# Optimization experiments

Hardware: AMD Instinct MI355X
Metric: run time of the kernel (lower is better)

Reference implementation:

```python
import jax, jax.numpy as jnp
import numpy as np

B, R, C, O, I = 256, 1152, 10, 16, 8  # batch, routes, digit caps, out dim, in dim


def conv2d(x, w, b, stride, pad):
    y = jax.lax.conv_general_dilated(
        x, w, (stride, stride), ((pad, pad), (pad, pad)),
        dimension_numbers=("NCHW", "OIHW", "NCHW"))
    return y + b[None, :, None, None]


def maxpool2(x):
    # kernel 2, stride 2, padding 1 (torch pads with -inf for max pool)
    return jax.lax.reduce_window(
        x, -jnp.inf, jax.lax.max,
        (1, 1, 2, 2), (1, 1, 2, 2), ((0, 0), (0, 0), (1, 1), (1, 1)))


def squash(t):
    sn = (t ** 2).sum(-1, keepdims=True)
    return sn * t / ((1.0 + sn) * jnp.sqrt(sn))


def setup_inputs() -> dict:
    key = jax.random.key(0)
    ks = jax.random.split(key, 8)
    return {
        "data": jax.random.normal(ks[0], (B, 3, 76, 76), dtype=jnp.float32),
        "conv1_w": jax.random.normal(ks[1], (64, 3, 3, 3), dtype=jnp.float32) * 0.1,
        "conv1_b": jnp.zeros((64,), jnp.float32),
        "conv2_w": jax.random.normal(ks[2], (128, 64, 3, 3), dtype=jnp.float32) * 0.05,
        "conv2_b": jnp.zeros((128,), jnp.float32),
        "prim_w": jax.random.normal(ks[3], (8, 32, 128, 9, 9), dtype=jnp.float32) * 0.02,
        "prim_b": jnp.zeros((8, 32), jnp.float32),
        "W": jax.random.normal(ks[4], (R, C, O, I), dtype=jnp.float32),
        "cls_w1": jax.random.normal(ks[5], (10, 160, 100), dtype=jnp.float32) * 0.05,
        "cls_b1": jnp.zeros((10, 100), jnp.float32),
        "cls_w2": jax.random.normal(ks[6], (10, 100, 1), dtype=jnp.float32) * 0.05,
        "cls_b2": jnp.zeros((10, 1), jnp.float32),
    }


def reference(data, conv1_w, conv1_b, conv2_w, conv2_b, prim_w, prim_b, W,
              cls_w1, cls_b1, cls_w2, cls_b2):
    # ---- ConvLayer ----
    x = jax.nn.relu(conv2d(data, conv1_w, conv1_b, 1, 0))   # [B,64,74,74]
    x = maxpool2(x)                                          # [B,64,38,38]
    x = jax.nn.relu(conv2d(x, conv2_w, conv2_b, 1, 1))       # [B,128,38,38]
    x = maxpool2(x)                                          # [B,128,20,20]

    # ---- PrimaryCaps: 8 parallel convs fused into one grouped-by-output conv ----
    pw = prim_w.reshape(8 * 32, 128, 9, 9)
    pb = prim_b.reshape(8 * 32)
    u = conv2d(x, pw, pb, 2, 0)                              # [B,256,6,6]
    u = u.reshape(B, R, I)                                   # [B,1152,8] (same flatten order as torch view)
    u = squash(u)

    # ---- DigitCaps dynamic routing ----
    u_hat = jnp.einsum("rcoi,bri->brco", W, u)               # [B,R,C,O]
    b_ij = jnp.zeros((R, C), u_hat.dtype)
    v_j = None
    for it in range(3):
        c_ij = jax.nn.softmax(b_ij, axis=0)                  # softmax over routes (dim=1 in torch)
        s_j = jnp.einsum("rc,brco->bco", c_ij, u_hat)        # [B,C,O]
        # torch squashes over trailing singleton dim -> elementwise squash
        v_j = squash(s_j[..., None])[..., 0]                 # [B,C,O]
        if it < 2:
            a_ij = jnp.einsum("brco,bco->brc", u_hat, v_j).mean(0)  # [R,C]
            b_ij = b_ij + a_ij

    output = v_j[..., None]                                  # [B,10,16,1]

    # ---- 10 classifiers (Linear->ReLU->Linear->Sigmoid), batched over classifier idx k ----
    feat = output.reshape(B, -1)                             # [B,160]
    h = jax.nn.relu(jnp.einsum("bf,kfh->bkh", feat, cls_w1) + cls_b1)
    logits = jnp.einsum("bkh,kho->bko", h, cls_w2) + cls_b2  # [B,10,1]
    cls = jax.nn.sigmoid(logits)[..., 0]                     # [B,10]
    return (output, cls)
```

## Files before the change

kernel.cpp:

```cpp
#include <hip/hip_runtime.h>
#include <hip/hip_bf16.h>


typedef __bf16 bf16x8 __attribute__((ext_vector_type(8)));
typedef float  f32x4  __attribute__((ext_vector_type(4)));
typedef ushort u16x8  __attribute__((ext_vector_type(8)));

static __device__ __forceinline__ ushort f2bf(float f) {
    __hip_bfloat16 h = __float2bfloat16(f);
    return *(ushort*)&h;
}
static __device__ __forceinline__ float b2f(ushort u) {
    return __uint_as_float(((unsigned)u) << 16);
}

__global__ __launch_bounds__(256) void k_prep_all(
    const float* __restrict__ w1, const float* __restrict__ w2,
    const float* __restrict__ pw, const float* __restrict__ W,
    __hip_bfloat16* __restrict__ Aw1, __hip_bfloat16* __restrict__ Aw2,
    __hip_bfloat16* __restrict__ Awt, __hip_bfloat16* __restrict__ Wt)
{
    int t = blockIdx.x * 256 + threadIdx.x;
    if (t < 2654208) {
        int oc = t / 10368, rem = t % 10368;
        int k81 = rem >> 7, ic = rem & 127;
        Awt[t] = __float2bfloat16(pw[(oc * 128 + ic) * 81 + k81]);
    } else if (t < 4128768) {
        int q = t - 2654208;
        int k = q / 160, co = q % 160;
        int r = k >> 3, i = k & 7, c = co >> 4, o = co & 15;
        Wt[q] = __float2bfloat16(W[(((size_t)r * 10 + c) * 16 + o) * 8 + i]);
    } else if (t < 4202496) {
        int q = t - 4128768;
        int oc = q / 576, rem = q % 576;
        int k9 = rem >> 6, ic = rem & 63;
        Aw2[q] = __float2bfloat16(w2[(oc * 64 + ic) * 9 + k9]);
    } else {
        int q = t - 4202496;
        int oc = q >> 5, k = q & 31;
        Aw1[q] = __float2bfloat16(k < 27 ? w1[oc * 27 + k] : 0.f);
    }
}

__global__ __launch_bounds__(256) void k_conv1_mfma(
    const float* __restrict__ data, const __hip_bfloat16* __restrict__ Aw1,
    const float* __restrict__ b1, __hip_bfloat16* __restrict__ P1t)
{
    __shared__ float tile[960];
    const int tid = threadIdx.x;
    const int py = blockIdx.x % 38, b = blockIdx.x / 38;

    #pragma unroll
    for (int c = 0; c < 4; c++) {
        int idx = tid + c * 256;
        if (idx < 960) {
            float val = 0.f;
            if (idx < 936) {
                int ic = idx / 312, rem = idx % 312;
                int rl = rem / 78, lc = rem % 78;
                int ri = 2 * py - 1 + rl, xi = lc - 1;
                if ((unsigned)ri < 76u && (unsigned)xi < 76u)
                    val = data[(b * 3 + ic) * 5776 + ri * 76 + xi];
            }
            tile[idx] = val;
        }
    }

    const int wave = tid >> 6, lane = tid & 63;
    const int l15 = lane & 15, quad = lane >> 4;

    bf16x8 af = *(const bf16x8*)((const ushort*)Aw1 + (wave * 16 + l15) * 32 + quad * 8);

    int koff[8]; bool kok[8];
    #pragma unroll
    for (int j = 0; j < 8; j++) {
        int kk = quad * 8 + j;
        kok[j] = kk < 27;
        int ic = kk / 9, rem = kk - ic * 9, ky = rem / 3, kx = rem - ky * 3;
        koff[j] = kok[j] ? (ic * 312 + ky * 78 + kx) : 0;
    }

    float bias[4];
    #pragma unroll
    for (int r = 0; r < 4; r++) bias[r] = b1[wave * 16 + quad * 4 + r];

    const bool valid0 = (py > 0);
    const bool valid1 = (py < 37);

    __syncthreads();

    #pragma unroll
    for (int t5 = 0; t5 < 5; t5++) {
        int n_x = t5 * 16 + l15;
        bool col_ok = (unsigned)(n_x - 1) < 74u;

        bf16x8 bf0, bf1;
        #pragma unroll
        for (int j = 0; j < 8; j++) {
            float v0 = tile[koff[j] + n_x];
            float v1 = tile[koff[j] + 78 + n_x];
            bool ok = col_ok && kok[j];
            bf0[j] = (__bf16)(ok ? v0 : 0.f);
            bf1[j] = (__bf16)(ok ? v1 : 0.f);
        }
        f32x4 z = {0.f, 0.f, 0.f, 0.f};
        f32x4 c0 = __builtin_amdgcn_mfma_f32_16x16x32_bf16(af, bf0, z, 0, 0, 0);
        f32x4 c1 = __builtin_amdgcn_mfma_f32_16x16x32_bf16(af, bf1, z, 0, 0, 0);

        f32x4 p;
        #pragma unroll
        for (int r = 0; r < 4; r++) {
            float r0 = (valid0 && col_ok) ? fmaxf(c0[r] + bias[r], 0.f) : 0.f;
            float r1 = (valid1 && col_ok) ? fmaxf(c1[r] + bias[r], 0.f) : 0.f;
            p[r] = fmaxf(r0, r1);
        }
        #pragma unroll
        for (int r = 0; r < 4; r++)
            p[r] = fmaxf(p[r], __shfl_xor(p[r], 1));

        if (!(l15 & 1)) {
            int px = t5 * 8 + (l15 >> 1);
            if (px < 38) {
                ushort4 pk;
                pk.x = f2bf(p[0]); pk.y = f2bf(p[1]);
                pk.z = f2bf(p[2]); pk.w = f2bf(p[3]);
                *(ushort4*)((ushort*)P1t + ((size_t)(b * 38 + py) * 38 + px) * 64
                            + wave * 16 + quad * 4) = pk;
            }
        }
    }
}

__global__ __launch_bounds__(512) void k_conv2_mfma(
    const __hip_bfloat16* __restrict__ P1t,
    const __hip_bfloat16* __restrict__ Aw2,
    const float* __restrict__ cb,
    __hip_bfloat16* __restrict__ Q)
{
    __shared__ ushort lA[128 * 72];
    __shared__ ushort lB[256 * 72];
    const int tid  = threadIdx.x;
    const int bn   = blockIdx.x;
    const int wave = tid >> 6, lane = tid & 63;
    const int wm   = wave & 1, wn = wave >> 1;
    const int lane15 = lane & 15, quad = lane >> 4;

    const int arow = tid >> 2, apart = tid & 3;
    const int brow = tid >> 1, bpart = tid & 1;

    int n = bn * 256 + brow;
    int b = n / 1444, yx = n % 1444;
    int y = yx / 38, x = yx % 38;

    const __hip_bfloat16* Abase = Aw2 + arow * 576;
    ushort* lAw = &lA[arow * 72 + apart * 16];
    ushort* lBw = &lB[brow * 72 + bpart * 32];
    const ushort* aRd = &lA[(wm * 64 + lane15) * 72 + quad * 8];
    const ushort* bRd = &lB[(wn * 64 + lane15) * 72 + quad * 8];

    f32x4 zero = {0.f, 0.f, 0.f, 0.f};
    f32x4 acc[4][4];
    #pragma unroll
    for (int i = 0; i < 4; i++)
        #pragma unroll
        for (int j = 0; j < 4; j++) acc[i][j] = zero;

    for (int kb = 0; kb < 9; kb++) {
        int ky = kb / 3, kx = kb - ky * 3;
        int iy = y + ky - 1, ix = x + kx - 1;
        bool ok = ((unsigned)iy < 38u) && ((unsigned)ix < 38u);

        const uint4* ga = (const uint4*)(Abase + kb * 64 + apart * 16);
        uint4 av0 = ga[0], av1 = ga[1];
        uint4 z4 = {0u, 0u, 0u, 0u};
        uint4 bv0 = z4, bv1 = z4, bv2 = z4, bv3 = z4;
        if (ok) {
            const uint4* gb = (const uint4*)(P1t + (((b * 38 + iy) * 38 + ix) << 6) + bpart * 32);
            bv0 = gb[0]; bv1 = gb[1]; bv2 = gb[2]; bv3 = gb[3];
        }

        __syncthreads();
        ((uint4*)lAw)[0] = av0; ((uint4*)lAw)[1] = av1;
        ((uint4*)lBw)[0] = bv0; ((uint4*)lBw)[1] = bv1;
        ((uint4*)lBw)[2] = bv2; ((uint4*)lBw)[3] = bv3;
        __syncthreads();

        #pragma unroll
        for (int kk = 0; kk < 2; kk++) {
            bf16x8 af[4], bf[4];
            #pragma unroll
            for (int tm = 0; tm < 4; tm++)
                af[tm] = *(const bf16x8*)(aRd + tm * 16 * 72 + kk * 32);
            #pragma unroll
            for (int tn = 0; tn < 4; tn++)
                bf[tn] = *(const bf16x8*)(bRd + tn * 16 * 72 + kk * 32);
            #pragma unroll
            for (int tm = 0; tm < 4; tm++)
                #pragma unroll
                for (int tn = 0; tn < 4; tn++)
                    acc[tm][tn] = __builtin_amdgcn_mfma_f32_16x16x32_bf16(
                        af[tm], bf[tn], acc[tm][tn], 0, 0, 0);
        }
    }

    #pragma unroll
    for (int tm = 0; tm < 4; tm++) {
        int m0 = wm * 64 + tm * 16 + quad * 4;
        float b0 = cb[m0], b1 = cb[m0 + 1], b2 = cb[m0 + 2], b3 = cb[m0 + 3];
        #pragma unroll
        for (int tn = 0; tn < 4; tn++) {
            int nn = bn * 256 + wn * 64 + tn * 16 + lane15;
            f32x4 a = acc[tm][tn];
            ushort4 pk;
            pk.x = f2bf(fmaxf(a[0] + b0, 0.f));
            pk.y = f2bf(fmaxf(a[1] + b1, 0.f));
            pk.z = f2bf(fmaxf(a[2] + b2, 0.f));
            pk.w = f2bf(fmaxf(a[3] + b3, 0.f));
            *(ushort4*)((ushort*)Q + (size_t)nn * 128 + m0) = pk;
        }
    }
}

__global__ __launch_bounds__(256) void k_pool2t(
    const __hip_bfloat16* __restrict__ Q, __hip_bfloat16* __restrict__ P2t)
{
    int t = blockIdx.x * 256 + threadIdx.x;
    int ic = t & 127, rest = t >> 7;
    int px = rest % 20, py = (rest / 20) % 20, b = rest / 400;
    float m = 0.f;
    #pragma unroll
    for (int dy = 0; dy < 2; dy++) {
        int y = 2 * py - 1 + dy;
        if ((unsigned)y >= 38u) continue;
        #pragma unroll
        for (int dx = 0; dx < 2; dx++) {
            int x = 2 * px - 1 + dx;
            if ((unsigned)x >= 38u) continue;
            m = fmaxf(m, __bfloat162float(Q[(((b * 38 + y) * 38 + x) << 7) + ic]));
        }
    }
    P2t[t] = __float2bfloat16(m);
}

__global__ __launch_bounds__(512) void k_primcaps_mfma(
    const __hip_bfloat16* __restrict__ P2t,
    const __hip_bfloat16* __restrict__ Awt,
    float* __restrict__ partU)
{
    __shared__ ushort lA[128 * 72];
    __shared__ ushort lB[256 * 72];
    const int tid  = threadIdx.x;
    const int chunk = blockIdx.x / 72;
    const int tile  = blockIdx.x % 72;
    const int bm   = tile & 1;
    const int bn   = tile >> 1;
    const int wave = tid >> 6, lane = tid & 63;
    const int wm   = wave & 1, wn = wave >> 1;
    const int lane15 = lane & 15, quad = lane >> 4;

    const int arow = tid >> 2, apart = tid & 3;
    const int brow = tid >> 1, bpart = tid & 1;

    int n  = bn * 256 + brow;
    int cb = n / 36, cs = n % 36;
    int cy = cs / 6, cx = cs % 6;
    const __hip_bfloat16* Bbase = P2t + ((cb * 20 + 2 * cy) * 20 + 2 * cx) * 128;
    const __hip_bfloat16* Abase = Awt + (bm * 128 + arow) * 10368;
    ushort* lAw = &lA[arow * 72 + apart * 16];
    ushort* lBw = &lB[brow * 72 + bpart * 32];
    const ushort* aRd = &lA[(wm * 64 + lane15) * 72 + quad * 8];
    const ushort* bRd = &lB[(wn * 64 + lane15) * 72 + quad * 8];

    f32x4 zero = {0.f, 0.f, 0.f, 0.f};
    f32x4 acc[4][4];
    #pragma unroll
    for (int i = 0; i < 4; i++)
        #pragma unroll
        for (int j = 0; j < 4; j++) acc[i][j] = zero;

    const int kb0 = chunk * 27;
    for (int ki = 0; ki < 27; ki++) {
        int kb = kb0 + ki;
        int k81 = kb >> 1;
        int ky = k81 / 9, kx = k81 - ky * 9;
        int goffA = kb * 64 + apart * 16;
        int goffB = (ky * 20 + kx) * 128 + (kb & 1) * 64 + bpart * 32;

        const uint4* ga = (const uint4*)(Abase + goffA);
        const uint4* gb = (const uint4*)(Bbase + goffB);
        uint4 av0 = ga[0], av1 = ga[1];
        uint4 bv0 = gb[0], bv1 = gb[1], bv2 = gb[2], bv3 = gb[3];

        __syncthreads();
        ((uint4*)lAw)[0] = av0; ((uint4*)lAw)[1] = av1;
        ((uint4*)lBw)[0] = bv0; ((uint4*)lBw)[1] = bv1;
        ((uint4*)lBw)[2] = bv2; ((uint4*)lBw)[3] = bv3;
        __syncthreads();

        #pragma unroll
        for (int kk = 0; kk < 2; kk++) {
            bf16x8 af[4], bf[4];
            #pragma unroll
            for (int tm = 0; tm < 4; tm++)
                af[tm] = *(const bf16x8*)(aRd + tm * 16 * 72 + kk * 32);
            #pragma unroll
            for (int tn = 0; tn < 4; tn++)
                bf[tn] = *(const bf16x8*)(bRd + tn * 16 * 72 + kk * 32);
            #pragma unroll
            for (int tm = 0; tm < 4; tm++)
                #pragma unroll
                for (int tn = 0; tn < 4; tn++)
                    acc[tm][tn] = __builtin_amdgcn_mfma_f32_16x16x32_bf16(
                        af[tm], bf[tn], acc[tm][tn], 0, 0, 0);
        }
    }

    float* base = partU + chunk * 2359296;
    #pragma unroll
    for (int tm = 0; tm < 4; tm++) {
        int m0 = bm * 128 + wm * 64 + tm * 16 + quad * 4;
        #pragma unroll
        for (int tn = 0; tn < 4; tn++) {
            int nn = bn * 256 + wn * 64 + tn * 16 + lane15;
            int ob = nn / 36, os = nn % 36;
            float* up = base + ob * 9216 + os;
            f32x4 a = acc[tm][tn];
            #pragma unroll
            for (int r = 0; r < 4; r++)
                up[(m0 + r) * 36] = a[r];
        }
    }
}

__global__ __launch_bounds__(256) void k_reduce_squash(
    const float* __restrict__ partU, const float* __restrict__ pb,
    ushort* __restrict__ u_bf)
{
    int t = blockIdx.x * 256 + threadIdx.x;
    float4 a = {0.f, 0.f, 0.f, 0.f}, b4 = {0.f, 0.f, 0.f, 0.f};
    #pragma unroll
    for (int p = 0; p < 6; p++) {
        const float4* pp = (const float4*)(partU + p * 2359296 + t * 8);
        float4 x = pp[0], y = pp[1];
        a.x += x.x; a.y += x.y; a.z += x.z; a.w += x.w;
        b4.x += y.x; b4.y += y.y; b4.z += y.z; b4.w += y.w;
    }
    int lb = (t % 1152) * 8;
    int oc0 = lb / 36, s0 = lb - oc0 * 36;
    float vals[8] = {a.x, a.y, a.z, a.w, b4.x, b4.y, b4.z, b4.w};
    float sn = 0.f;
    #pragma unroll
    for (int e = 0; e < 8; e++) {
        int oc = oc0 + ((s0 + e) >= 36 ? 1 : 0);
        vals[e] += pb[oc];
        sn += vals[e] * vals[e];
    }
    float sc = sqrtf(sn) / (1.f + sn);
    u16x8 o8;
    #pragma unroll
    for (int e = 0; e < 8; e++) o8[e] = f2bf(vals[e] * sc);
    *(u16x8*)(u_bf + (size_t)t * 8) = o8;
}

__global__ __launch_bounds__(320) void k_sj_fused(
    const ushort* __restrict__ u_bf,
    const __hip_bfloat16* __restrict__ Wt,
    const float* __restrict__ expb,
    float* __restrict__ partS,
    int iter)
{
    __shared__ ushort ush[8 * 1152];
    __shared__ float cf[1440];
    __shared__ float sred[320];
    __shared__ float sinv[10];
    const int tid = threadIdx.x;
    const int bt = blockIdx.x & 31, kc = blockIdx.x >> 5;
    const int co = tid % 160, half = tid / 160;

    if (iter > 0) {
        int c = tid % 10, g = tid / 10;
        float s = 0.f;
        for (int r = g; r < 1152; r += 32) s += expb[r * 10 + c];
        sred[tid] = s;
        for (int i = tid; i < 1440; i += 320) cf[i] = expb[kc * 1440 + i];
        __syncthreads();
        if (tid < 10) {
            float t2 = 0.f;
            #pragma unroll
            for (int gg = 0; gg < 32; gg++) t2 += sred[tid + gg * 10];
            sinv[tid] = 1.f / t2;
        }
    }
    for (int i = tid; i < 1152; i += 320)
        ((uint4*)ush)[i] = ((const uint4*)u_bf)[(size_t)(bt * 8 + (i / 144)) * 1152
                                                + kc * 144 + (i % 144)];
    __syncthreads();

    const int cc = co >> 4;
    const float scl = (iter > 0) ? sinv[cc] : 0.f;
    const float cuni = 1.f / 1152.f;
    const ushort* wp = (const ushort*)Wt + ((size_t)kc * 1152 + half * 576) * 160 + co;

    float acc[8] = {0.f, 0.f, 0.f, 0.f, 0.f, 0.f, 0.f, 0.f};
    for (int rr = 0; rr < 72; rr++) {
        float cl = (iter == 0) ? cuni : cf[(half * 72 + rr) * 10 + cc] * scl;
        float wv[8];
        #pragma unroll
        for (int ii = 0; ii < 8; ii++)
            wv[ii] = b2f(wp[(rr * 8 + ii) * 160]) * cl;
        int kbase = half * 576 + rr * 8;
        #pragma unroll
        for (int bb = 0; bb < 8; bb++) {
            u16x8 uq = *(const u16x8*)&ush[bb * 1152 + kbase];
            #pragma unroll
            for (int ii = 0; ii < 8; ii++)
                acc[bb] += wv[ii] * b2f(uq[ii]);
        }
    }
    float* ps = partS + (kc * 2 + half) * 40960;
    #pragma unroll
    for (int bb = 0; bb < 8; bb++)
        ps[(bt * 8 + bb) * 160 + co] = acc[bb];
}

__global__ __launch_bounds__(320) void k_vj_cls(
    const float* __restrict__ partS, float* __restrict__ v,
    const float* __restrict__ w1, const float* __restrict__ b1,
    const float* __restrict__ w2, const float* __restrict__ b2,
    float* __restrict__ out, int write_out)
{
    const int b = blockIdx.x;
    const int tid = threadIdx.x;
    __shared__ float feat[160];
    if (tid < 160) {
        float s = 0.f;
        #pragma unroll
        for (int p = 0; p < 16; p++) s += partS[p * 40960 + b * 160 + tid];
        float vv = s * fabsf(s) / (1.f + s * s);
        v[b * 160 + tid] = vv;
        feat[tid] = vv;
        if (write_out) out[b * 160 + tid] = vv;
    }
    if (!write_out) return;
    __syncthreads();
    int k = tid >> 5, j = tid & 31;
    float acc = 0.f;
    for (int h = j; h < 100; h += 32) {
        float a = b1[k * 100 + h];
        for (int f = 0; f < 160; f++) a += feat[f] * w1[(k * 160 + f) * 100 + h];
        acc += fmaxf(a, 0.f) * w2[k * 100 + h];
    }
    #pragma unroll
    for (int d = 16; d > 0; d >>= 1) acc += __shfl_xor(acc, d);
    if (j == 0)
        out[40960 + b * 10 + k] = 1.f / (1.f + expf(-(acc + b2[k])));
}

__global__ __launch_bounds__(320) void k_mmat_aij(
    const ushort* __restrict__ u_bf, const float* __restrict__ v,
    const float* __restrict__ W, float* __restrict__ bij,
    float* __restrict__ expb)
{
    const int r = blockIdx.x;
    const int tid = threadIdx.x;
    const int co = tid % 160, bh = tid / 160;
    float acc[8] = {0.f, 0.f, 0.f, 0.f, 0.f, 0.f, 0.f, 0.f};
    for (int b = bh; b < 256; b += 2) {
        float vv = v[b * 160 + co];
        u16x8 uq = *(const u16x8*)(u_bf + (size_t)b * 9216 + r * 8);
        #pragma unroll
        for (int j = 0; j < 8; j++) acc[j] += vv * b2f(uq[j]);
    }
    __shared__ float red[2560];
    __shared__ float Ml[8][160];
    #pragma unroll
    for (int j = 0; j < 8; j++) red[j * 320 + bh * 160 + co] = acc[j];
    __syncthreads();
    if (tid < 160) {
        #pragma unroll
        for (int j = 0; j < 8; j++)
            Ml[j][tid] = (red[j * 320 + tid] + red[j * 320 + 160 + tid]) * (1.f / 256.f);
    }
    __syncthreads();
    int c = tid >> 5, j32 = tid & 31;
    const float* wr = W + ((size_t)r * 10 + c) * 128;
    float a2 = 0.f;
    #pragma unroll
    for (int m = 0; m < 4; m++) {
        int idx = j32 + m * 32;
        int o = idx >> 3, i = idx & 7;
        a2 += wr[idx] * Ml[i][c * 16 + o];
    }
    #pragma unroll
    for (int d = 16; d > 0; d >>= 1) a2 += __shfl_xor(a2, d);
    if (j32 == 0) {
        float nb = bij[c * 1152 + r] + a2;
        bij[c * 1152 + r] = nb;
        expb[r * 10 + c] = expf(nb);
    }
}

extern "C" void kernel_launch(void* const* d_in, const int* in_sizes, int n_in,
                              void* d_out, int out_size, void* d_ws, size_t ws_size,
                              hipStream_t stream) {
    const float* data    = (const float*)d_in[0];
    const float* conv1_w = (const float*)d_in[1];
    const float* conv1_b = (const float*)d_in[2];
    const float* conv2_w = (const float*)d_in[3];
    const float* conv2_b = (const float*)d_in[4];
    const float* prim_w  = (const float*)d_in[5];
    const float* prim_b  = (const float*)d_in[6];
    const float* W       = (const float*)d_in[7];
    const float* cls_w1  = (const float*)d_in[8];
    const float* cls_b1  = (const float*)d_in[9];
    const float* cls_w2  = (const float*)d_in[10];
    const float* cls_b2  = (const float*)d_in[11];
    float* out = (float*)d_out;

    char* ws = (char*)d_ws;
    __hip_bfloat16* Q     = (__hip_bfloat16*)(ws + 0);
    float*          partU = (float*)(ws + 0);
    __hip_bfloat16* P1t   = (__hip_bfloat16*)(ws + 94633984);
    __hip_bfloat16* P2t   = (__hip_bfloat16*)(ws + 94633984);
    __hip_bfloat16* Awt   = (__hip_bfloat16*)(ws + 141950976);
    __hip_bfloat16* Wt    = (__hip_bfloat16*)(ws + 147259392);
    ushort*         u_bf  = (ushort*)(ws + 150208512);
    float*          partS = (float*)(ws + 154927104);
    float*          v     = (float*)(ws + 163446784);
    float*          bij   = (float*)(ws + 163610624);
    float*          expb  = (float*)(ws + 163656704);
    __hip_bfloat16* Aw2   = (__hip_bfloat16*)(ws + 163702784);
    __hip_bfloat16* Aw1   = (__hip_bfloat16*)(ws + 163850240);

    hipMemsetAsync(bij, 0, 11520 * sizeof(float), stream);

    k_prep_all<<<16424, 256, 0, stream>>>(conv1_w, conv2_w, prim_w, W,
                                          Aw1, Aw2, Awt, Wt);
    k_conv1_mfma<<<9728, 256, 0, stream>>>(data, Aw1, conv1_b, P1t);
    k_conv2_mfma<<<1444, 512, 0, stream>>>(P1t, Aw2, conv2_b, Q);
    k_pool2t<<<51200, 256, 0, stream>>>(Q, P2t);
    k_primcaps_mfma<<<432, 512, 0, stream>>>(P2t, Awt, partU);
    k_reduce_squash<<<1152, 256, 0, stream>>>(partU, prim_b, u_bf);

    for (int it = 0; it < 3; it++) {
        k_sj_fused<<<256, 320, 0, stream>>>(u_bf, Wt, expb, partS, it);
        k_vj_cls<<<256, 320, 0, stream>>>(partS, v, cls_w1, cls_b1, cls_w2,
                                          cls_b2, out, it == 2 ? 1 : 0);
        if (it < 2)
            k_mmat_aij<<<1152, 320, 0, stream>>>(u_bf, v, W, bij, expb);
    }
}
```

Baseline: 613.2 us.

## Fuse maxpool into conv2 MFMA epilogue via pool-ordered output pixels

Reorders conv2's output-pixel enumeration so each group of four adjacent lanes covers one 2x2 pool window (including padded positions), then does max pooling in the epilogue with lane shuffles and writes the pooled P2t directly. This removes the separate pool kernel and the full-resolution intermediate Q write and read. In exchange it computes conv outputs for padded positions (1600 vs 1444 tiles per 4 images, about 11% extra MFMA work), and input gathers become less contiguous.

```diff
diff --git a/kernel.cpp b/kernel.cpp
--- a/kernel.cpp
+++ b/kernel.cpp
@@ -131,16 +131,16 @@
     }
 }
 
-__global__ __launch_bounds__(512) void k_conv2_mfma(
+__global__ __launch_bounds__(512) void k_conv2_pool_mfma(
     const __hip_bfloat16* __restrict__ P1t,
     const __hip_bfloat16* __restrict__ Aw2,
     const float* __restrict__ cb,
-    __hip_bfloat16* __restrict__ Q)
+    __hip_bfloat16* __restrict__ P2t)
 {
     __shared__ ushort lA[128 * 72];
     __shared__ ushort lB[256 * 72];
     const int tid  = threadIdx.x;
-    const int bn   = blockIdx.x;
+    const int grp  = blockIdx.x / 25, toff = blockIdx.x % 25;
     const int wave = tid >> 6, lane = tid & 63;
     const int wm   = wave & 1, wn = wave >> 1;
     const int lane15 = lane & 15, quad = lane >> 4;
@@ -148,9 +148,12 @@
     const int arow = tid >> 2, apart = tid & 3;
     const int brow = tid >> 1, bpart = tid & 1;
 
-    int n = bn * 256 + brow;
-    int b = n / 1444, yx = n % 1444;
-    int y = yx / 38, x = yx % 38;
+    int off = toff * 256 + brow;
+    int bb = off / 1600, rem = off % 1600;
+    int cell = rem >> 2, q = rem & 3;
+    int py = cell / 20, px = cell % 20;
+    int y = 2 * py - 1 + (q >> 1), x = 2 * px - 1 + (q & 1);
+    int b = grp * 4 + bb;
 
     const __hip_bfloat16* Abase = Aw2 + arow * 576;
     ushort* lAw = &lA[arow * 72 + apart * 16];
@@ -204,42 +207,35 @@
     }
 
     #pragma unroll
-    for (int tm = 0; tm < 4; tm++) {
-        int m0 = wm * 64 + tm * 16 + quad * 4;
-        float b0 = cb[m0], b1 = cb[m0 + 1], b2 = cb[m0 + 2], b3 = cb[m0 + 3];
-        #pragma unroll
-        for (int tn = 0; tn < 4; tn++) {
-            int nn = bn * 256 + wn * 64 + tn * 16 + lane15;
+    for (int tn = 0; tn < 4; tn++) {
+        int woff = toff * 256 + wn * 64 + tn * 16 + lane15;
+        int ebb = woff / 1600, erem = woff % 1600;
+        int ecell = erem >> 2, eq = erem & 3;
+        int epy = ecell / 20, epx = ecell % 20;
+        int ey = 2 * epy - 1 + (eq >> 1), ex = 2 * epx - 1 + (eq & 1);
+        bool vq = ((unsigned)ey < 38u) && ((unsigned)ex < 38u);
+        int eb = grp * 4 + ebb;
+        #pragma unroll
+        for (int tm = 0; tm < 4; tm++) {
+            int m0 = wm * 64 + tm * 16 + quad * 4;
             f32x4 a = acc[tm][tn];
-            ushort4 pk;
-            pk.x = f2bf(fmaxf(a[0] + b0, 0.f));
-            pk.y = f2bf(fmaxf(a[1] + b1, 0.f));
-            pk.z = f2bf(fmaxf(a[2] + b2, 0.f));
-            pk.w = f2bf(fmaxf(a[3] + b3, 0.f));
-            *(ushort4*)((ushort*)Q + (size_t)nn * 128 + m0) = pk;
-        }
-    }
-}
-
-__global__ __launch_bounds__(256) void k_pool2t(
-    const __hip_bfloat16* __restrict__ Q, __hip_bfloat16* __restrict__ P2t)
-{
-    int t = blockIdx.x * 256 + threadIdx.x;
-    int ic = t & 127, rest = t >> 7;
-    int px = rest % 20, py = (rest / 20) % 20, b = rest / 400;
-    float m = 0.f;
-    #pragma unroll
-    for (int dy = 0; dy < 2; dy++) {
-        int y = 2 * py - 1 + dy;
-        if ((unsigned)y >= 38u) continue;
-        #pragma unroll
-        for (int dx = 0; dx < 2; dx++) {
-            int x = 2 * px - 1 + dx;
-            if ((unsigned)x >= 38u) continue;
-            m = fmaxf(m, __bfloat162float(Q[(((b * 38 + y) * 38 + x) << 7) + ic]));
-        }
-    }
-    P2t[t] = __float2bfloat16(m);
+            f32x4 p;
+            #pragma unroll
+            for (int r = 0; r < 4; r++)
+                p[r] = vq ? fmaxf(a[r] + cb[m0 + r], 0.f) : 0.f;
+            #pragma unroll
+            for (int r = 0; r < 4; r++) {
+                p[r] = fmaxf(p[r], __shfl_xor(p[r], 1));
+                p[r] = fmaxf(p[r], __shfl_xor(p[r], 2));
+            }
+            if (eq == 0) {
+                ushort4 pk;
+                pk.x = f2bf(p[0]); pk.y = f2bf(p[1]);
+                pk.z = f2bf(p[2]); pk.w = f2bf(p[3]);
+                *(ushort4*)((ushort*)P2t + (((size_t)eb * 20 + epy) * 20 + epx) * 128 + m0) = pk;
+            }
+        }
+    }
 }
 
 __global__ __launch_bounds__(512) void k_primcaps_mfma(
@@ -518,10 +514,9 @@
     float* out = (float*)d_out;
 
     char* ws = (char*)d_ws;
-    __hip_bfloat16* Q     = (__hip_bfloat16*)(ws + 0);
     float*          partU = (float*)(ws + 0);
+    __hip_bfloat16* P2t   = (__hip_bfloat16*)(ws + 56623104);
     __hip_bfloat16* P1t   = (__hip_bfloat16*)(ws + 94633984);
-    __hip_bfloat16* P2t   = (__hip_bfloat16*)(ws + 94633984);
     __hip_bfloat16* Awt   = (__hip_bfloat16*)(ws + 141950976);
     __hip_bfloat16* Wt    = (__hip_bfloat16*)(ws + 147259392);
     ushort*         u_bf  = (ushort*)(ws + 150208512);
@@ -537,8 +532,7 @@
     k_prep_all<<<16424, 256, 0, stream>>>(conv1_w, conv2_w, prim_w, W,
                                           Aw1, Aw2, Awt, Wt);
     k_conv1_mfma<<<9728, 256, 0, stream>>>(data, Aw1, conv1_b, P1t);
-    k_conv2_mfma<<<1444, 512, 0, stream>>>(P1t, Aw2, conv2_b, Q);
-    k_pool2t<<<51200, 256, 0, stream>>>(Q, P2t);
+    k_conv2_pool_mfma<<<1600, 512, 0, stream>>>(P1t, Aw2, conv2_b, P2t);
     k_primcaps_mfma<<<432, 512, 0, stream>>>(P2t, Awt, partU);
     k_reduce_squash<<<1152, 256, 0, stream>>>(partU, prim_b, u_bf);
 
```

Result: faster. 590.5 us (-3.7%).
